# Optimization experiments

Measured on AMD Instinct MI355X. Metric: run time of the kernel, lower is better.

Reference implementation:

```python
import jax, jax.numpy as jnp
import numpy as np

EMBED_DIM = 1024
B, S = 4, 2048


def setup_inputs() -> dict:
    key = jax.random.key(0)
    ks = jax.random.split(key, 7)
    D = EMBED_DIM
    lim = 1.0 / np.sqrt(D)  # torch nn.Linear default init range
    inp = {
        "input": jax.random.normal(ks[0], (B, S, D), dtype=jnp.float32),
        "Wq": jax.random.uniform(ks[1], (D, D), jnp.float32, -lim, lim),
        "bq": jax.random.uniform(ks[2], (D,), jnp.float32, -lim, lim),
        "Wk": jax.random.uniform(ks[3], (D, D), jnp.float32, -lim, lim),
        "bk": jax.random.uniform(ks[4], (D,), jnp.float32, -lim, lim),
        "Wv": jax.random.uniform(ks[5], (D, D), jnp.float32, -lim, lim),
        "bv": jax.random.uniform(ks[6], (D,), jnp.float32, -lim, lim),
    }
    return inp


def reference(input, Wq, bq, Wk, bk, Wv, bv):
    # Linear layers: x @ W^T + b (torch convention: W is [out, in])
    q = jnp.einsum("bsd,ed->bse", input, Wq) + bq
    k = jnp.einsum("bsd,ed->bse", input, Wk) + bk
    v = jnp.einsum("bsd,ed->bse", input, Wv) + bv
    scale = 1.0 / jnp.sqrt(jnp.float32(EMBED_DIM))
    # [B, S, S] similarity matrix (unfused, matches original)
    similarity = jnp.einsum("bqd,bkd->bqk", q, k) * scale
    attention = jax.nn.softmax(similarity, axis=-1)
    return jnp.einsum("bqk,bkd->bqd", attention, v)
```

## Files before the change

### kernel.cpp

```cpp
#include <hip/hip_runtime.h>


typedef unsigned short ushort_t;
typedef __bf16 bf16x8 __attribute__((ext_vector_type(8)));
typedef float f32x4 __attribute__((ext_vector_type(4)));

__device__ __forceinline__ unsigned short f2bf(float f) {
  unsigned u = __builtin_bit_cast(unsigned, f);
  u += 0x7fffu + ((u >> 16) & 1u);
  return (unsigned short)(u >> 16);
}

template<int MODE, int RX, int RY>
__global__ __launch_bounds__(512, 4)
void gemm128(const ushort_t* __restrict__ A, long long sAz, int lda,
             const ushort_t* __restrict__ Bm, long long sBz, int ldb,
             void* __restrict__ C0, void* __restrict__ C1, void* __restrict__ C2,
             long long sCz, int ldc, int K, float scale, const float* __restrict__ bias)
{
  constexpr int SLOT = 8192;
  constexpr int BUF  = 2 * SLOT;
  __shared__ ushort_t lds_[2 * BUF] __attribute__((aligned(16)));

  constexpr int BPR = RX * RY;
  const int gx = gridDim.x;
  const int lin = blockIdx.y * gx + blockIdx.x;
  const int xcd = lin & 7, s = lin >> 3;
  const int chunk = s / BPR, idx = s % BPR;
  const int rect = chunk * 8 + xcd;
  const int nrx = gx / RX;
  const int bx = (rect % nrx) * RX + (idx % RX);
  const int by = (rect / nrx) * RY + (idx / RX);

  const int z = blockIdx.z;
  const ushort_t* Ab = A  + (long long)z * sAz + (long long)by * 128 * lda;
  const ushort_t* Bb = Bm + (long long)z * sBz + (long long)bx * 128 * ldb;

  const int tid = threadIdx.x, wid = tid >> 6, lane = tid & 63;
  const int wr = wid >> 2, wc = wid & 3;
  const int l15 = lane & 15;
  const int kx0 = (((lane >> 4) + 0) ^ (l15 & 7)) * 8;
  const int kx1 = (((lane >> 4) + 4) ^ (l15 & 7)) * 8;
  const int srow = lane >> 3;
  const int scol = ((lane & 7) ^ (srow & 7)) * 8;

  auto stg = [&](int mat, int q, int t) {
    const ushort_t* g0 = (mat == 0 ? Ab : Bb);
    const int ld = (mat == 0 ? lda : ldb);
#pragma unroll
    for (int j = 0; j < 2; ++j) {
      const ushort_t* g = g0 + (long long)(j * 64 + wid * 8 + srow) * ld + t * 64 + scol;
      __builtin_amdgcn_global_load_lds(
          (const __attribute__((address_space(1))) void*)g,
          (__attribute__((address_space(3))) void*)
            (&lds_[q * BUF + mat * SLOT + (j * 64 + wid * 8) * 64]),
          16, 0, 0);
    }
  };

  f32x4 acc[4][2];
#pragma unroll
  for (int m = 0; m < 4; ++m)
#pragma unroll
    for (int n = 0; n < 2; ++n)
#pragma unroll
      for (int j = 0; j < 4; ++j) acc[m][n][j] = 0.f;

  stg(0, 0, 0); stg(1, 0, 0); stg(0, 1, 1);
  asm volatile("s_waitcnt vmcnt(2)" ::: "memory");
  __builtin_amdgcn_s_barrier();

  const int NT = K >> 6;
  bf16x8 a0[4], a1[4], bf[2];

  for (int t = 0; t < NT; ++t) {
    const int q = t & 1;
    const ushort_t* Al = &lds_[q * BUF] + wr * 64 * 64;
    const ushort_t* Bl = &lds_[q * BUF + SLOT] + wc * 32 * 64;

#pragma unroll
    for (int m = 0; m < 4; ++m) a0[m] = *(const bf16x8*)(Al + (m * 16 + l15) * 64 + kx0);
#pragma unroll
    for (int n = 0; n < 2; ++n) bf[n] = *(const bf16x8*)(Bl + (n * 16 + l15) * 64 + kx0);
#pragma unroll
    for (int m = 0; m < 4; ++m) a1[m] = *(const bf16x8*)(Al + (m * 16 + l15) * 64 + kx1);
    __builtin_amdgcn_sched_barrier(0);
    if (t + 1 < NT) stg(1, q ^ 1, t + 1);
    __builtin_amdgcn_s_barrier();
    __builtin_amdgcn_s_setprio(1);
#pragma unroll
    for (int m = 0; m < 4; ++m)
#pragma unroll
      for (int n = 0; n < 2; ++n)
        acc[m][n] = __builtin_amdgcn_mfma_f32_16x16x32_bf16(a0[m], bf[n], acc[m][n], 0, 0, 0);
    __builtin_amdgcn_s_setprio(0);
    __builtin_amdgcn_s_barrier();

#pragma unroll
    for (int n = 0; n < 2; ++n) bf[n] = *(const bf16x8*)(Bl + (n * 16 + l15) * 64 + kx1);
    __builtin_amdgcn_sched_barrier(0);
    if (t + 2 < NT) stg(0, q, t + 2);
    __builtin_amdgcn_s_barrier();
    __builtin_amdgcn_s_setprio(1);
#pragma unroll
    for (int m = 0; m < 4; ++m)
#pragma unroll
      for (int n = 0; n < 2; ++n)
        acc[m][n] = __builtin_amdgcn_mfma_f32_16x16x32_bf16(a1[m], bf[n], acc[m][n], 0, 0, 0);
    __builtin_amdgcn_s_setprio(0);
    if (t < NT - 2)       asm volatile("s_waitcnt vmcnt(2)" ::: "memory");
    else if (t == NT - 2) asm volatile("s_waitcnt vmcnt(0)" ::: "memory");
    __builtin_amdgcn_s_barrier();
  }

  const int r4 = (lane >> 4) * 4;
  const long long crow0 = (long long)by * 128 + wr * 64;
  const int ccol0 = bx * 128 + wc * 32;

  if constexpr (MODE == 0) {
#pragma unroll
    for (int n = 0; n < 2; ++n) {
      const int cg = ccol0 + n * 16 + l15;
#pragma unroll
      for (int m = 0; m < 4; ++m)
#pragma unroll
        for (int j = 0; j < 4; ++j) {
          const long long rg = crow0 + m * 16 + r4 + j;
          ((float*)C0)[(long long)z * sCz + rg * ldc + cg] = acc[m][n][j] * scale;
        }
    }
  } else {
    const int sel = ccol0 >> 10;
#pragma unroll
    for (int n = 0; n < 2; ++n) {
      const int cg = ccol0 + n * 16 + l15;
      const int col = cg & 1023;
      const float badd = bias[cg];
      if (sel < 2) {
        ushort_t* outp = (ushort_t*)(sel == 0 ? C0 : C1);
#pragma unroll
        for (int m = 0; m < 4; ++m)
#pragma unroll
          for (int j = 0; j < 4; ++j) {
            const long long rg = crow0 + m * 16 + r4 + j;
            outp[rg * 1024 + col] = f2bf(acc[m][n][j] + badd);
          }
      } else {
        ushort_t* vt = (ushort_t*)C2;
#pragma unroll
        for (int m = 0; m < 4; ++m) {
          const long long rg = crow0 + m * 16 + r4;
          const long long b = rg >> 11, srw = rg & 2047;
          ushort4 o;
          o.x = f2bf(acc[m][n][0] + badd);
          o.y = f2bf(acc[m][n][1] + badd);
          o.z = f2bf(acc[m][n][2] + badd);
          o.w = f2bf(acc[m][n][3] + badd);
          *(ushort4*)&vt[b * 2097152 + (long long)col * 2048 + srw] = o;
        }
      }
    }
  }
}

__global__ __launch_bounds__(512, 1)
void gemm256(const ushort_t* __restrict__ A, long long sAz, int lda,
             const ushort_t* __restrict__ Bm, long long sBz, int ldb,
             float* __restrict__ C, long long sCz, int ldc,
             int K, float scale)
{
  constexpr int AH = 8192, BH = 8192, BUF = 2 * AH + 2 * BH;
  constexpr int RX = 4, RY = 2, BPR = RX * RY;
  __shared__ ushort_t lds_[2 * BUF] __attribute__((aligned(16)));

  const int gx = gridDim.x;
  const int lin = blockIdx.y * gx + blockIdx.x;
  const int xcd = lin & 7, s = lin >> 3;
  const int chunk = s / BPR, idx = s % BPR;
  const int rect = chunk * 8 + xcd;
  const int nrx = gx / RX;
  const int bx = (rect % nrx) * RX + (idx % RX);
  const int by = (rect / nrx) * RY + (idx / RX);

  const int z = blockIdx.z;
  const ushort_t* Ab = A  + (long long)z * sAz + (long long)by * 256 * lda;
  const ushort_t* Bb = Bm + (long long)z * sBz + (long long)bx * 256 * ldb;

  const int tid = threadIdx.x, wid = tid >> 6, lane = tid & 63;
  const int wr = wid >> 2, wc = wid & 3;
  const int l15 = lane & 15;
  const int kx0 = (((lane >> 4) + 0) ^ (l15 & 7)) * 8;
  const int kx1 = (((lane >> 4) + 4) ^ (l15 & 7)) * 8;
  const int srow = lane >> 3;
  const int scol = ((lane & 7) ^ (srow & 7)) * 8;

  auto stgA = [&](int q, int h, int t) {
#pragma unroll
    for (int j = 0; j < 2; ++j) {
      const ushort_t* g = Ab + (long long)(h * 128 + wid * 16 + j * 8 + srow) * lda
                             + t * 64 + scol;
      __builtin_amdgcn_global_load_lds(
          (const __attribute__((address_space(1))) void*)g,
          (__attribute__((address_space(3))) void*)
            (&lds_[q * BUF + h * AH + (wid * 128 + j * 64) * 8]),
          16, 0, 0);
    }
  };
  auto stgB = [&](int q, int h, int t) {
#pragma unroll
    for (int j = 0; j < 2; ++j) {
      const ushort_t* g = Bb + (long long)(h * 128 + wid * 16 + j * 8 + srow) * ldb
                             + t * 64 + scol;
      __builtin_amdgcn_global_load_lds(
          (const __attribute__((address_space(1))) void*)g,
          (__attribute__((address_space(3))) void*)
            (&lds_[q * BUF + 2 * AH + h * BH + (wid * 128 + j * 64) * 8]),
          16, 0, 0);
    }
  };

  f32x4 acc[8][4];
#pragma unroll
  for (int m = 0; m < 8; ++m)
#pragma unroll
    for (int n = 0; n < 4; ++n)
#pragma unroll
      for (int j = 0; j < 4; ++j) acc[m][n][j] = 0.f;

  stgA(0, 0, 0); stgA(0, 1, 0);
  stgB(0, 0, 0); stgB(0, 1, 0);
  stgA(1, 0, 1); stgA(1, 1, 1);
  asm volatile("s_waitcnt vmcnt(4)" ::: "memory");
  __builtin_amdgcn_s_barrier();

  const int NT = K >> 6;
  bf16x8 af[4], bf[4];

  for (int t = 0; t < NT; ++t) {
    const int q = t & 1;
    const ushort_t* Al = &lds_[q * BUF + wr * AH];
    const ushort_t* Bl = &lds_[q * BUF + 2 * AH + (wc >> 1) * BH + (wc & 1) * 4096];

#pragma unroll
    for (int n = 0; n < 4; ++n) bf[n] = *(const bf16x8*)(Bl + (n * 16 + l15) * 64 + kx0);
#pragma unroll
    for (int m = 0; m < 4; ++m) af[m] = *(const bf16x8*)(Al + (m * 16 + l15) * 64 + kx0);
    if (t + 1 < NT) stgB(q ^ 1, 0, t + 1);
    __builtin_amdgcn_s_barrier();
    __builtin_amdgcn_s_setprio(1);
#pragma unroll
    for (int m = 0; m < 4; ++m)
#pragma unroll
      for (int n = 0; n < 4; ++n)
        acc[m][n] = __builtin_amdgcn_mfma_f32_16x16x32_bf16(af[m], bf[n], acc[m][n], 0, 0, 0);
    __builtin_amdgcn_s_setprio(0);
    __builtin_amdgcn_s_barrier();

#pragma unroll
    for (int m = 0; m < 4; ++m) af[m] = *(const bf16x8*)(Al + ((4 + m) * 16 + l15) * 64 + kx0);
    if (t + 1 < NT) stgB(q ^ 1, 1, t + 1);
    __builtin_amdgcn_s_barrier();
    __builtin_amdgcn_s_setprio(1);
#pragma unroll
    for (int m = 0; m < 4; ++m)
#pragma unroll
      for (int n = 0; n < 4; ++n)
        acc[4 + m][n] = __builtin_amdgcn_mfma_f32_16x16x32_bf16(af[m], bf[n], acc[4 + m][n], 0, 0, 0);
    __builtin_amdgcn_s_setprio(0);
    __builtin_amdgcn_s_barrier();

#pragma unroll
    for (int n = 0; n < 4; ++n) bf[n] = *(const bf16x8*)(Bl + (n * 16 + l15) * 64 + kx1);
#pragma unroll
    for (int m = 0; m < 4; ++m) af[m] = *(const bf16x8*)(Al + (m * 16 + l15) * 64 + kx1);
    __builtin_amdgcn_s_barrier();
    __builtin_amdgcn_s_setprio(1);
#pragma unroll
    for (int m = 0; m < 4; ++m)
#pragma unroll
      for (int n = 0; n < 4; ++n)
        acc[m][n] = __builtin_amdgcn_mfma_f32_16x16x32_bf16(af[m], bf[n], acc[m][n], 0, 0, 0);
    __builtin_amdgcn_s_setprio(0);
    __builtin_amdgcn_s_barrier();

#pragma unroll
    for (int m = 0; m < 4; ++m) af[m] = *(const bf16x8*)(Al + ((4 + m) * 16 + l15) * 64 + kx1);
    __builtin_amdgcn_sched_barrier(0);
    if (t + 2 < NT) { stgA(q, 0, t + 2); stgA(q, 1, t + 2); }
    __builtin_amdgcn_s_barrier();
    __builtin_amdgcn_s_setprio(1);
#pragma unroll
    for (int m = 0; m < 4; ++m)
#pragma unroll
      for (int n = 0; n < 4; ++n)
        acc[4 + m][n] = __builtin_amdgcn_mfma_f32_16x16x32_bf16(af[m], bf[n], acc[4 + m][n], 0, 0, 0);
    __builtin_amdgcn_s_setprio(0);
    if (t < NT - 2)       asm volatile("s_waitcnt vmcnt(4)" ::: "memory");
    else if (t == NT - 2) asm volatile("s_waitcnt vmcnt(0)" ::: "memory");
    __builtin_amdgcn_s_barrier();
  }

  const int r4 = (lane >> 4) * 4;
  const long long crow0 = (long long)by * 256 + wr * 128;
  const int ccol0 = bx * 256 + wc * 64;
#pragma unroll
  for (int n = 0; n < 4; ++n) {
    const int cg = ccol0 + n * 16 + l15;
#pragma unroll
    for (int m = 0; m < 8; ++m)
#pragma unroll
      for (int j = 0; j < 4; ++j) {
        const long long rg = crow0 + m * 16 + r4 + j;
        C[(long long)z * sCz + rg * ldc + cg] = acc[m][n][j] * scale;
      }
  }
}

__global__ __launch_bounds__(256)
void cast_f32_bf16(const float* __restrict__ in, ushort_t* __restrict__ out, long long n)
{
  long long i = ((long long)blockIdx.x * blockDim.x + threadIdx.x) * 4;
  const long long stride = (long long)gridDim.x * blockDim.x * 4;
  for (; i < n; i += stride) {
    const float4 v = *(const float4*)&in[i];
    ushort4 o;
    o.x = f2bf(v.x); o.y = f2bf(v.y); o.z = f2bf(v.z); o.w = f2bf(v.w);
    *(ushort4*)&out[i] = o;
  }
}

__global__ __launch_bounds__(256)
void prep_w(const float* __restrict__ Wq, const float* __restrict__ Wk,
            const float* __restrict__ Wv, const float* __restrict__ bq,
            const float* __restrict__ bk, const float* __restrict__ bv,
            ushort_t* __restrict__ w3, float* __restrict__ bcat)
{
  const int which = blockIdx.x >> 10;
  const float* W = (which == 0) ? Wq : (which == 1) ? Wk : Wv;
  const long long i = ((long long)(blockIdx.x & 1023) * 256 + threadIdx.x) * 4;
  const float4 v = *(const float4*)&W[i];
  ushort4 o;
  o.x = f2bf(v.x); o.y = f2bf(v.y); o.z = f2bf(v.z); o.w = f2bf(v.w);
  *(ushort4*)&w3[(long long)which * 1024 * 1024 + i] = o;
  const int g = blockIdx.x * 256 + threadIdx.x;
  if (g < 3072) bcat[g] = (g < 1024) ? bq[g] : (g < 2048) ? bk[g - 1024] : bv[g - 2048];
}

__global__ __launch_bounds__(256)
void softmax2048(const float* __restrict__ Sc, ushort_t* __restrict__ P)
{
  const long long row = blockIdx.x;
  const float* s = Sc + row * 2048;
  const int tid = threadIdx.x;
  const int wave = tid >> 6, lane = tid & 63;

  const float4 a = *(const float4*)&s[tid * 4];
  const float4 b = *(const float4*)&s[1024 + tid * 4];
  float m = fmaxf(fmaxf(fmaxf(a.x, a.y), fmaxf(a.z, a.w)),
                  fmaxf(fmaxf(b.x, b.y), fmaxf(b.z, b.w)));
#pragma unroll
  for (int off = 32; off > 0; off >>= 1) m = fmaxf(m, __shfl_xor(m, off));
  __shared__ float redm[4], reds[4];
  if (lane == 0) redm[wave] = m;
  __syncthreads();
  m = fmaxf(fmaxf(redm[0], redm[1]), fmaxf(redm[2], redm[3]));

  float e[8];
  e[0] = __expf(a.x - m); e[1] = __expf(a.y - m); e[2] = __expf(a.z - m); e[3] = __expf(a.w - m);
  e[4] = __expf(b.x - m); e[5] = __expf(b.y - m); e[6] = __expf(b.z - m); e[7] = __expf(b.w - m);
  float sum = ((e[0] + e[1]) + (e[2] + e[3])) + ((e[4] + e[5]) + (e[6] + e[7]));
#pragma unroll
  for (int off = 32; off > 0; off >>= 1) sum += __shfl_xor(sum, off);
  if (lane == 0) reds[wave] = sum;
  __syncthreads();
  sum = (reds[0] + reds[1]) + (reds[2] + reds[3]);
  const float inv = 1.0f / sum;

  ushort4 o;
  o.x = f2bf(e[0] * inv); o.y = f2bf(e[1] * inv); o.z = f2bf(e[2] * inv); o.w = f2bf(e[3] * inv);
  *(ushort4*)&P[row * 2048 + tid * 4] = o;
  o.x = f2bf(e[4] * inv); o.y = f2bf(e[5] * inv); o.z = f2bf(e[6] * inv); o.w = f2bf(e[7] * inv);
  *(ushort4*)&P[row * 2048 + 1024 + tid * 4] = o;
}

extern "C" void kernel_launch(void* const* d_in, const int* in_sizes, int n_in,
                              void* d_out, int out_size, void* d_ws, size_t ws_size,
                              hipStream_t stream)
{
  constexpr int B = 4, S = 2048, D = 1024;
  constexpr long long MT = (long long)B * S;
  constexpr long long SD = (long long)S * D;
  constexpr long long SS = (long long)S * S;

  const float* x  = (const float*)d_in[0];
  const float* Wq = (const float*)d_in[1];
  const float* bq = (const float*)d_in[2];
  const float* Wk = (const float*)d_in[3];
  const float* bk = (const float*)d_in[4];
  const float* Wv = (const float*)d_in[5];
  const float* bv = (const float*)d_in[6];
  float* out = (float*)d_out;

  char* base = (char*)d_ws;
  ushort_t* q      = (ushort_t*)(base);
  ushort_t* k      = (ushort_t*)(base + 16777216);
  ushort_t* vt     = (ushort_t*)(base + 33554432);
  float*    scores = (float*)   (base + 50331648);
  ushort_t* P      = (ushort_t*)(base + 117440512);
  ushort_t* xb     = (ushort_t*)(base + 50331648);
  ushort_t* w3     = (ushort_t*)(base + 67108864);
  float*    bcat   = (float*)   (base + 73400320);

  cast_f32_bf16<<<2048, 256, 0, stream>>>(x, xb, MT * D);
  prep_w<<<3072, 256, 0, stream>>>(Wq, Wk, Wv, bq, bk, bv, w3, bcat);

  gemm128<2, 4, 8><<<dim3(24, 64, 1), 512, 0, stream>>>(
      xb, 0, D, w3, 0, D, q, k, vt, 0, 1024, D, 1.f, bcat);

  gemm256<<<dim3(8, 8, 4), 512, 0, stream>>>(
      q, SD, D, k, SD, D, scores, SS, S, D, 0.03125f);

  softmax2048<<<MT, 256, 0, stream>>>(scores, P);

  gemm128<0, 2, 4><<<dim3(8, 16, 4), 512, 0, stream>>>(
      P, SS, S, vt, (long long)D * S, S, out, nullptr, nullptr, SD, D, S, 1.f, nullptr);
}
```

Baseline: 175.8 us.

## Store attention scores in fp16 and restructure GEMM load staging

The score GEMM now writes fp16 instead of fp32, and softmax reads fp16 with 8-wide vector loads and stores. This halves the traffic of the largest intermediate buffer. Both GEMM kernels change their prefetch schedule so A and B for step t+2 are issued together after an lgkmcnt wait, using incremented base pointers. The vmcnt waits are adjusted to match, and workspace offsets move so the fp16 scores do not alias xb and w3. The fp16 scores reduce precision of the logits before softmax, and the new schedule changes how load latency overlaps the MFMA work.

```diff
diff --git a/kernel.cpp b/kernel.cpp
--- a/kernel.cpp
+++ b/kernel.cpp
@@ -4,6 +4,8 @@
 typedef unsigned short ushort_t;
 typedef __bf16 bf16x8 __attribute__((ext_vector_type(8)));
 typedef float f32x4 __attribute__((ext_vector_type(4)));
+typedef _Float16 h8 __attribute__((ext_vector_type(8)));
+typedef short short8v __attribute__((ext_vector_type(8)));
 
 __device__ __forceinline__ unsigned short f2bf(float f) {
   unsigned u = __builtin_bit_cast(unsigned, f);
@@ -44,18 +46,19 @@
   const int srow = lane >> 3;
   const int scol = ((lane & 7) ^ (srow & 7)) * 8;
 
-  auto stg = [&](int mat, int q, int t) {
-    const ushort_t* g0 = (mat == 0 ? Ab : Bb);
-    const int ld = (mat == 0 ? lda : ldb);
-#pragma unroll
-    for (int j = 0; j < 2; ++j) {
-      const ushort_t* g = g0 + (long long)(j * 64 + wid * 8 + srow) * ld + t * 64 + scol;
+  const ushort_t* agA = Ab + (long long)(wid * 8 + srow) * lda + scol;
+  const ushort_t* agB = Bb + (long long)(wid * 8 + srow) * ldb + scol;
+  const long long jA = (long long)64 * lda, jB = (long long)64 * ldb;
+  const int ldsA0 = wid * 512;
+  const int ldsB0 = SLOT + wid * 512;
+
+  auto stage = [&](const ushort_t* g, long long jstep, int ldsOff) {
+#pragma unroll
+    for (int j = 0; j < 2; ++j)
       __builtin_amdgcn_global_load_lds(
-          (const __attribute__((address_space(1))) void*)g,
-          (__attribute__((address_space(3))) void*)
-            (&lds_[q * BUF + mat * SLOT + (j * 64 + wid * 8) * 64]),
+          (const __attribute__((address_space(1))) void*)(g + j * jstep),
+          (__attribute__((address_space(3))) void*)(&lds_[ldsOff + j * 4096]),
           16, 0, 0);
-    }
   };
 
   f32x4 acc[4][2];
@@ -66,8 +69,11 @@
 #pragma unroll
       for (int j = 0; j < 4; ++j) acc[m][n][j] = 0.f;
 
-  stg(0, 0, 0); stg(1, 0, 0); stg(0, 1, 1);
-  asm volatile("s_waitcnt vmcnt(2)" ::: "memory");
+  stage(agA, jA, 0 * BUF + ldsA0); agA += 64;
+  stage(agB, jB, 0 * BUF + ldsB0); agB += 64;
+  stage(agA, jA, 1 * BUF + ldsA0); agA += 64;
+  stage(agB, jB, 1 * BUF + ldsB0); agB += 64;
+  asm volatile("s_waitcnt vmcnt(4)" ::: "memory");
   __builtin_amdgcn_s_barrier();
 
   const int NT = K >> 6;
@@ -75,8 +81,8 @@
 
   for (int t = 0; t < NT; ++t) {
     const int q = t & 1;
-    const ushort_t* Al = &lds_[q * BUF] + wr * 64 * 64;
-    const ushort_t* Bl = &lds_[q * BUF + SLOT] + wc * 32 * 64;
+    const ushort_t* Al = &lds_[q * BUF] + wr * 4096;
+    const ushort_t* Bl = &lds_[q * BUF + SLOT] + wc * 2048;
 
 #pragma unroll
     for (int m = 0; m < 4; ++m) a0[m] = *(const bf16x8*)(Al + (m * 16 + l15) * 64 + kx0);
@@ -84,8 +90,6 @@
     for (int n = 0; n < 2; ++n) bf[n] = *(const bf16x8*)(Bl + (n * 16 + l15) * 64 + kx0);
 #pragma unroll
     for (int m = 0; m < 4; ++m) a1[m] = *(const bf16x8*)(Al + (m * 16 + l15) * 64 + kx1);
-    __builtin_amdgcn_sched_barrier(0);
-    if (t + 1 < NT) stg(1, q ^ 1, t + 1);
     __builtin_amdgcn_s_barrier();
     __builtin_amdgcn_s_setprio(1);
 #pragma unroll
@@ -98,8 +102,12 @@
 
 #pragma unroll
     for (int n = 0; n < 2; ++n) bf[n] = *(const bf16x8*)(Bl + (n * 16 + l15) * 64 + kx1);
+    asm volatile("s_waitcnt lgkmcnt(0)" ::: "memory");
     __builtin_amdgcn_sched_barrier(0);
-    if (t + 2 < NT) stg(0, q, t + 2);
+    if (t + 2 < NT) {
+      stage(agA, jA, q * BUF + ldsA0); agA += 64;
+      stage(agB, jB, q * BUF + ldsB0); agB += 64;
+    }
     __builtin_amdgcn_s_barrier();
     __builtin_amdgcn_s_setprio(1);
 #pragma unroll
@@ -108,7 +116,7 @@
       for (int n = 0; n < 2; ++n)
         acc[m][n] = __builtin_amdgcn_mfma_f32_16x16x32_bf16(a1[m], bf[n], acc[m][n], 0, 0, 0);
     __builtin_amdgcn_s_setprio(0);
-    if (t < NT - 2)       asm volatile("s_waitcnt vmcnt(2)" ::: "memory");
+    if (t < NT - 2)       asm volatile("s_waitcnt vmcnt(4)" ::: "memory");
     else if (t == NT - 2) asm volatile("s_waitcnt vmcnt(0)" ::: "memory");
     __builtin_amdgcn_s_barrier();
   }
@@ -166,7 +174,7 @@
 __global__ __launch_bounds__(512, 1)
 void gemm256(const ushort_t* __restrict__ A, long long sAz, int lda,
              const ushort_t* __restrict__ Bm, long long sBz, int ldb,
-             float* __restrict__ C, long long sCz, int ldc,
+             _Float16* __restrict__ C, long long sCz, int ldc,
              int K, float scale)
 {
   constexpr int AH = 8192, BH = 8192, BUF = 2 * AH + 2 * BH;
@@ -194,29 +202,30 @@
   const int srow = lane >> 3;
   const int scol = ((lane & 7) ^ (srow & 7)) * 8;
 
-  auto stgA = [&](int q, int h, int t) {
-#pragma unroll
-    for (int j = 0; j < 2; ++j) {
-      const ushort_t* g = Ab + (long long)(h * 128 + wid * 16 + j * 8 + srow) * lda
-                             + t * 64 + scol;
-      __builtin_amdgcn_global_load_lds(
-          (const __attribute__((address_space(1))) void*)g,
-          (__attribute__((address_space(3))) void*)
-            (&lds_[q * BUF + h * AH + (wid * 128 + j * 64) * 8]),
-          16, 0, 0);
-    }
+  const ushort_t* agA = Ab + (long long)(wid * 16 + srow) * lda + scol;
+  const ushort_t* agB = Bb + (long long)(wid * 16 + srow) * ldb + scol;
+
+  auto stageA = [&](int q) {
+#pragma unroll
+    for (int h = 0; h < 2; ++h)
+#pragma unroll
+      for (int j = 0; j < 2; ++j)
+        __builtin_amdgcn_global_load_lds(
+            (const __attribute__((address_space(1))) void*)(agA + (long long)(h * 128 + j * 8) * lda),
+            (__attribute__((address_space(3))) void*)
+              (&lds_[q * BUF + h * AH + (wid * 128 + j * 64) * 8]),
+            16, 0, 0);
   };
-  auto stgB = [&](int q, int h, int t) {
-#pragma unroll
-    for (int j = 0; j < 2; ++j) {
-      const ushort_t* g = Bb + (long long)(h * 128 + wid * 16 + j * 8 + srow) * ldb
-                             + t * 64 + scol;
-      __builtin_amdgcn_global_load_lds(
-          (const __attribute__((address_space(1))) void*)g,
-          (__attribute__((address_space(3))) void*)
-            (&lds_[q * BUF + 2 * AH + h * BH + (wid * 128 + j * 64) * 8]),
-          16, 0, 0);
-    }
+  auto stageB = [&](int q) {
+#pragma unroll
+    for (int h = 0; h < 2; ++h)
+#pragma unroll
+      for (int j = 0; j < 2; ++j)
+        __builtin_amdgcn_global_load_lds(
+            (const __attribute__((address_space(1))) void*)(agB + (long long)(h * 128 + j * 8) * ldb),
+            (__attribute__((address_space(3))) void*)
+              (&lds_[q * BUF + 2 * AH + h * BH + (wid * 128 + j * 64) * 8]),
+            16, 0, 0);
   };
 
   f32x4 acc[8][4];
@@ -227,10 +236,9 @@
 #pragma unroll
       for (int j = 0; j < 4; ++j) acc[m][n][j] = 0.f;
 
-  stgA(0, 0, 0); stgA(0, 1, 0);
-  stgB(0, 0, 0); stgB(0, 1, 0);
-  stgA(1, 0, 1); stgA(1, 1, 1);
-  asm volatile("s_waitcnt vmcnt(4)" ::: "memory");
+  stageA(0); stageB(0); agA += 64; agB += 64;
+  stageA(1); stageB(1); agA += 64; agB += 64;
+  asm volatile("s_waitcnt vmcnt(8)" ::: "memory");
   __builtin_amdgcn_s_barrier();
 
   const int NT = K >> 6;
@@ -245,7 +253,6 @@
     for (int n = 0; n < 4; ++n) bf[n] = *(const bf16x8*)(Bl + (n * 16 + l15) * 64 + kx0);
 #pragma unroll
     for (int m = 0; m < 4; ++m) af[m] = *(const bf16x8*)(Al + (m * 16 + l15) * 64 + kx0);
-    if (t + 1 < NT) stgB(q ^ 1, 0, t + 1);
     __builtin_amdgcn_s_barrier();
     __builtin_amdgcn_s_setprio(1);
 #pragma unroll
@@ -258,7 +265,6 @@
 
 #pragma unroll
     for (int m = 0; m < 4; ++m) af[m] = *(const bf16x8*)(Al + ((4 + m) * 16 + l15) * 64 + kx0);
-    if (t + 1 < NT) stgB(q ^ 1, 1, t + 1);
     __builtin_amdgcn_s_barrier();
     __builtin_amdgcn_s_setprio(1);
 #pragma unroll
@@ -285,8 +291,9 @@
 
 #pragma unroll
     for (int m = 0; m < 4; ++m) af[m] = *(const bf16x8*)(Al + ((4 + m) * 16 + l15) * 64 + kx1);
+    asm volatile("s_waitcnt lgkmcnt(0)" ::: "memory");
     __builtin_amdgcn_sched_barrier(0);
-    if (t + 2 < NT) { stgA(q, 0, t + 2); stgA(q, 1, t + 2); }
+    if (t + 2 < NT) { stageA(q); stageB(q); agA += 64; agB += 64; }
     __builtin_amdgcn_s_barrier();
     __builtin_amdgcn_s_setprio(1);
 #pragma unroll
@@ -295,7 +302,7 @@
       for (int n = 0; n < 4; ++n)
         acc[4 + m][n] = __builtin_amdgcn_mfma_f32_16x16x32_bf16(af[m], bf[n], acc[4 + m][n], 0, 0, 0);
     __builtin_amdgcn_s_setprio(0);
-    if (t < NT - 2)       asm volatile("s_waitcnt vmcnt(4)" ::: "memory");
+    if (t < NT - 2)       asm volatile("s_waitcnt vmcnt(8)" ::: "memory");
     else if (t == NT - 2) asm volatile("s_waitcnt vmcnt(0)" ::: "memory");
     __builtin_amdgcn_s_barrier();
   }
@@ -311,7 +318,7 @@
 #pragma unroll
       for (int j = 0; j < 4; ++j) {
         const long long rg = crow0 + m * 16 + r4 + j;
-        C[(long long)z * sCz + rg * ldc + cg] = acc[m][n][j] * scale;
+        C[(long long)z * sCz + rg * ldc + cg] = (_Float16)(acc[m][n][j] * scale);
       }
   }
 }
@@ -347,17 +354,19 @@
 }
 
 __global__ __launch_bounds__(256)
-void softmax2048(const float* __restrict__ Sc, ushort_t* __restrict__ P)
+void softmax2048(const _Float16* __restrict__ Sc, ushort_t* __restrict__ P)
 {
   const long long row = blockIdx.x;
-  const float* s = Sc + row * 2048;
+  const _Float16* s = Sc + row * 2048;
   const int tid = threadIdx.x;
   const int wave = tid >> 6, lane = tid & 63;
 
-  const float4 a = *(const float4*)&s[tid * 4];
-  const float4 b = *(const float4*)&s[1024 + tid * 4];
-  float m = fmaxf(fmaxf(fmaxf(a.x, a.y), fmaxf(a.z, a.w)),
-                  fmaxf(fmaxf(b.x, b.y), fmaxf(b.z, b.w)));
+  const h8 a = *(const h8*)&s[tid * 8];
+  float f[8];
+#pragma unroll
+  for (int i = 0; i < 8; ++i) f[i] = (float)a[i];
+  float m = fmaxf(fmaxf(fmaxf(f[0], f[1]), fmaxf(f[2], f[3])),
+                  fmaxf(fmaxf(f[4], f[5]), fmaxf(f[6], f[7])));
 #pragma unroll
   for (int off = 32; off > 0; off >>= 1) m = fmaxf(m, __shfl_xor(m, off));
   __shared__ float redm[4], reds[4];
@@ -366,8 +375,8 @@
   m = fmaxf(fmaxf(redm[0], redm[1]), fmaxf(redm[2], redm[3]));
 
   float e[8];
-  e[0] = __expf(a.x - m); e[1] = __expf(a.y - m); e[2] = __expf(a.z - m); e[3] = __expf(a.w - m);
-  e[4] = __expf(b.x - m); e[5] = __expf(b.y - m); e[6] = __expf(b.z - m); e[7] = __expf(b.w - m);
+#pragma unroll
+  for (int i = 0; i < 8; ++i) e[i] = __expf(f[i] - m);
   float sum = ((e[0] + e[1]) + (e[2] + e[3])) + ((e[4] + e[5]) + (e[6] + e[7]));
 #pragma unroll
   for (int off = 32; off > 0; off >>= 1) sum += __shfl_xor(sum, off);
@@ -376,11 +385,10 @@
   sum = (reds[0] + reds[1]) + (reds[2] + reds[3]);
   const float inv = 1.0f / sum;
 
-  ushort4 o;
-  o.x = f2bf(e[0] * inv); o.y = f2bf(e[1] * inv); o.z = f2bf(e[2] * inv); o.w = f2bf(e[3] * inv);
-  *(ushort4*)&P[row * 2048 + tid * 4] = o;
-  o.x = f2bf(e[4] * inv); o.y = f2bf(e[5] * inv); o.z = f2bf(e[6] * inv); o.w = f2bf(e[7] * inv);
-  *(ushort4*)&P[row * 2048 + 1024 + tid * 4] = o;
+  short8v o;
+#pragma unroll
+  for (int i = 0; i < 8; ++i) o[i] = (short)f2bf(e[i] * inv);
+  *(short8v*)&P[row * 2048 + tid * 8] = o;
 }
 
 extern "C" void kernel_launch(void* const* d_in, const int* in_sizes, int n_in,
@@ -402,14 +410,14 @@
   float* out = (float*)d_out;
 
   char* base = (char*)d_ws;
-  ushort_t* q      = (ushort_t*)(base);
-  ushort_t* k      = (ushort_t*)(base + 16777216);
-  ushort_t* vt     = (ushort_t*)(base + 33554432);
-  float*    scores = (float*)   (base + 50331648);
-  ushort_t* P      = (ushort_t*)(base + 117440512);
-  ushort_t* xb     = (ushort_t*)(base + 50331648);
-  ushort_t* w3     = (ushort_t*)(base + 67108864);
-  float*    bcat   = (float*)   (base + 73400320);
+  ushort_t*  q       = (ushort_t*)(base);
+  ushort_t*  k       = (ushort_t*)(base + 16777216);
+  ushort_t*  vt      = (ushort_t*)(base + 33554432);
+  _Float16*  scores  = (_Float16*)(base + 50331648);
+  ushort_t*  P       = (ushort_t*)(base + 117440512);
+  ushort_t*  xb      = (ushort_t*)(base + 83886080);
+  ushort_t*  w3      = (ushort_t*)(base + 100663296);
+  float*     bcat    = (float*)   (base + 106954752);
 
   cast_f32_bf16<<<2048, 256, 0, stream>>>(x, xb, MT * D);
   prep_w<<<3072, 256, 0, stream>>>(Wq, Wk, Wv, bq, bk, bv, w3, bcat);
```

After: 168.6 us. -4.1%, faster.
